# Optimization experiments

Hardware: AMD Instinct MI355X
Metric: run time of the kernel (lower is better)

The kernel has to match this reference:

```python
import jax, jax.numpy as jnp
import numpy as np

IN_F, ASS, OUT_F = 1024, 100000, 1024
P = 0.0005
NUM_ROUNDS = 24  # fixed replacement for the data-dependent convergence loop
TOTAL = IN_F + ASS + OUT_F


def _build_graph(seed=0):
    """Random digraph: input->assoc and assoc->(assoc|out) with prob P,
    plus guaranteed edges so the propagation_check of the original passes
    (every assoc node reachable, every output has an in-edge)."""
    rng = np.random.default_rng(seed)
    ass0, out0 = IN_F, IN_F + ASS
    n_ie = int(P * IN_F * ASS)
    ie_src = rng.integers(0, IN_F, n_ie)
    ie_dst = rng.integers(ass0, out0, n_ie)
    n_ae = int(P * ASS * (ASS + OUT_F))
    ae_src = rng.integers(ass0, out0, n_ae)
    ae_dst = rng.integers(ass0, out0 + OUT_F, n_ae)
    # guarantee reachability: assoc node j gets an in-edge from a random node < j
    g_dst = np.arange(ass0, out0)
    g_src = (rng.random(ASS) * g_dst).astype(np.int64)
    gi = g_src < IN_F
    ie_src = np.concatenate([ie_src, g_src[gi]])
    ie_dst = np.concatenate([ie_dst, g_dst[gi]])
    ae_src = np.concatenate([ae_src, g_src[~gi]])
    ae_dst = np.concatenate([ae_dst, g_dst[~gi]])
    # every output neuron gets at least one in-edge from a random assoc
    ae_src = np.concatenate([ae_src, rng.integers(ass0, out0, OUT_F)])
    ae_dst = np.concatenate([ae_dst, np.arange(out0, out0 + OUT_F)])
    return ie_src, ie_dst, ae_src, ae_dst


def setup_inputs() -> dict:
    key = jax.random.key(0)
    k1, k2, k3 = jax.random.split(key, 3)
    ie_src, ie_dst, ae_src, ae_dst = _build_graph()
    x = jax.random.normal(k1, (1, IN_F), jnp.float32)
    # nn.init.uniform_(w, -1, 1)
    input_weights = jax.random.uniform(k2, (len(ie_src),), jnp.float32, -1.0, 1.0)
    assoc_weights = jax.random.uniform(k3, (len(ae_src),), jnp.float32, -1.0, 1.0)
    return {
        'x': x,
        'input_weights': input_weights,
        'assoc_weights': assoc_weights,
        'in_edge_src': jnp.asarray(ie_src, jnp.int32),
        'in_edge_dst': jnp.asarray(ie_dst, jnp.int32),
        'ass_edge_src': jnp.asarray(ae_src, jnp.int32),
        'ass_edge_dst': jnp.asarray(ae_dst, jnp.int32),
    }


def _forward(x, input_weights, assoc_weights, in_edge_src, in_edge_dst,
             ass_edge_src, ass_edge_dst):
    idx = jnp.arange(TOTAL)
    is_assoc = (idx >= IN_F) & (idx < IN_F + ASS)
    # --- input phase: each input neuron i sends x[i]*w along its out-edges ---
    msgs = x[0][in_edge_src] * input_weights              # [E_in]
    mem = jax.ops.segment_sum(msgs, in_edge_dst, num_segments=TOTAL)
    recv = jax.ops.segment_sum(jnp.ones_like(in_edge_dst), in_edge_dst,
                               num_segments=TOTAL) > 0
    status = jnp.where(recv, 1, 0).astype(jnp.int32)      # 0=inactive,1=working,2=activated

    # --- synchronous wave propagation through associative neurons ---
    def step(carry, _):
        mem, status = carry
        fire = (status == 1) & is_assoc                    # working assoc neurons fire
        src_fire = fire[ass_edge_src]
        # forward_fn(memory, w) = activation(sum(memory)) * w  (tanh activation)
        vals = jnp.where(src_fire, jnp.tanh(mem[ass_edge_src]) * assoc_weights, 0.0)
        delta = jax.ops.segment_sum(vals, ass_edge_dst, num_segments=TOTAL)
        got = jax.ops.segment_sum(src_fire.astype(jnp.int32), ass_edge_dst,
                                  num_segments=TOTAL) > 0
        mem = jnp.where(fire, 0.0, mem) + delta            # fired neurons erase memory
        status = jnp.where(fire, 2, jnp.where(got & (status == 0), 1, status))
        return (mem, status), None

    (mem, status), _ = jax.lax.scan(step, (mem, status), None, length=NUM_ROUNDS)
    # --- output phase: Y[i] = activation(sum(memory)) * 1 ---
    return jnp.tanh(mem[IN_F + ASS:])


def reference(x, input_weights, assoc_weights, in_edge_src, in_edge_dst,
              ass_edge_src, ass_edge_dst):
    return _forward(x, input_weights, assoc_weights, in_edge_src, in_edge_dst,
                    ass_edge_src, ass_edge_dst)
```

## Files before the change

kernel.cpp:

```cpp
#include <hip/hip_runtime.h>

#define IN_F 1024
#define ASS 100000
#define OUT_F 1024
#define TOTAL (IN_F + ASS + OUT_F)
#define ASS0 IN_F
#define OUT0 (IN_F + ASS)
#define NDST (ASS + OUT_F)
#define NUM_ROUNDS 24

#define BIN_SZ 1024
#define BIN_SH 10
#define BIN_MK 1023
#define NBINS ((NDST + BIN_SZ - 1) / BIN_SZ)
#define NCON 512
#define CON_T 1024
#define SPLIT 8
#define NBM32 3136
#define TAIL_R 8

typedef int i4v __attribute__((ext_vector_type(4)));
typedef float f4v __attribute__((ext_vector_type(4)));
typedef unsigned int u2v __attribute__((ext_vector_type(2)));


__global__ __launch_bounds__(256) void kz(float* mem, u2v* ltv, int* flags,
                                          int* binA, int* binR, int* scur,
                                          unsigned* bm, int cap, int scap) {
  int i = blockIdx.x * 256 + threadIdx.x;
  int gs = gridDim.x * 256;
  u2v init;
  init.x = 255u;
  init.y = 0u;
  for (int k = i; k < TOTAL; k += gs) {
    mem[k] = 0.f;
    ltv[k] = init;
  }
  for (int k = i; k < NBINS; k += gs) {
    binA[k] = k * cap;
    binR[k] = (k + 1) * cap;
    scur[k] = k * scap;
  }
  for (int k = i; k < NBM32; k += gs) bm[k] = 0u;
  if (i < 32) flags[i] = 0;
}

__global__ __launch_bounds__(256) void ki(const float* __restrict__ x,
                                          const float* __restrict__ iw,
                                          const int* __restrict__ ies,
                                          const int* __restrict__ ied, int E_in,
                                          float* mem, unsigned int* ltv_raw,
                                          unsigned* bm) {
  int e = blockIdx.x * 256 + threadIdx.x;
  if (e < E_in) {
    int d = ied[e];
    atomicAdd(&mem[d], x[ies[e]] * iw[e]);
    ltv_raw[2 * d] = 0u;
    int b = d - ASS0;
    atomicOr(&bm[b >> 5], 1u << (b & 31));
  }
}

__global__ __launch_bounds__(CON_T) void kc(const int* __restrict__ aes,
                                            const int* __restrict__ aed,
                                            const float* __restrict__ aw,
                                            int E_a, int* binA, int* binR,
                                            const unsigned* __restrict__ bm,
                                            u2v* __restrict__ csr, float* mem,
                                            u2v* ltv) {
  for (int i = blockIdx.x * CON_T + (int)threadIdx.x; i < ASS;
       i += NCON * CON_T) {
    int node = ASS0 + i;
    u2v lt = ltv[node];
    if (lt.x == 0u) {
      lt.y = __float_as_uint(tanhf(mem[node]));
      ltv[node] = lt;
      mem[node] = 0.f;
    }
  }
  __shared__ unsigned sbm[NBM32];
  __shared__ int hA[2][NBINS], hR[2][NBINS];
  __shared__ int cA[NBINS], cR[NBINS];
  for (int k = threadIdx.x; k < NBM32; k += CON_T) sbm[k] = bm[k];
  for (int b = threadIdx.x; b < NBINS; b += CON_T) {
    hA[0][b] = 0;
    hA[1][b] = 0;
    hR[0][b] = 0;
    hR[1][b] = 0;
  }
  __syncthreads();
  int cp = (threadIdx.x >> 6) & 1;
  const i4v* aed4 = (const i4v*)aed;
  const i4v* aes4 = (const i4v*)aes;
  const f4v* aw4 = (const f4v*)aw;
  int nv4 = E_a >> 2;
  int chunk4 = (nv4 + NCON - 1) / NCON;
  int v0 = blockIdx.x * chunk4;
  int v1 = min(v0 + chunk4, nv4);
  int bv = v0 + (int)threadIdx.x;

  i4v dr0, dr1, dr2, sr0, sr1, sr2;
#pragma unroll
  for (int k = 0; k < 3; ++k) {
    int v = bv + k * CON_T;
    if (v < v1) {
      i4v d4 = aed4[v];
      i4v s4 = aes4[v];
      if (k == 0) { dr0 = d4; sr0 = s4; }
      if (k == 1) { dr1 = d4; sr1 = s4; }
      if (k == 2) { dr2 = d4; sr2 = s4; }
#pragma unroll
      for (int j = 0; j < 4; ++j) {
        int b = (d4[j] - ASS0) >> BIN_SH;
        int si = s4[j] - ASS0;
        bool a0 = (sbm[si >> 5] >> (si & 31)) & 1u;
        atomicAdd(a0 ? &hA[cp][b] : &hR[cp][b], 1);
      }
    }
  }
  for (int v = bv + 3 * CON_T; v < v1; v += CON_T) {
    i4v d4 = aed4[v];
    i4v s4 = aes4[v];
#pragma unroll
    for (int j = 0; j < 4; ++j) {
      int b = (d4[j] - ASS0) >> BIN_SH;
      int si = s4[j] - ASS0;
      bool a0 = (sbm[si >> 5] >> (si & 31)) & 1u;
      atomicAdd(a0 ? &hA[cp][b] : &hR[cp][b], 1);
    }
  }
  if (blockIdx.x == 0) {
    for (int e = (nv4 << 2) + (int)threadIdx.x; e < E_a; e += CON_T) {
      int b = (aed[e] - ASS0) >> BIN_SH;
      int si = aes[e] - ASS0;
      bool a0 = (sbm[si >> 5] >> (si & 31)) & 1u;
      atomicAdd(a0 ? &hA[cp][b] : &hR[cp][b], 1);
    }
  }
  __syncthreads();
  for (int b = threadIdx.x; b < NBINS; b += CON_T) {
    int ca = hA[0][b] + hA[1][b];
    int cr = hR[0][b] + hR[1][b];
    cA[b] = ca ? atomicAdd(&binA[b], ca) : 0;
    cR[b] = cr ? (atomicSub(&binR[b], cr) - cr) : 0;
  }
  __syncthreads();
#pragma unroll
  for (int k = 0; k < 3; ++k) {
    int v = bv + k * CON_T;
    if (v < v1) {
      i4v d4 = (k == 0) ? dr0 : (k == 1) ? dr1 : dr2;
      i4v s4 = (k == 0) ? sr0 : (k == 1) ? sr1 : sr2;
      f4v w4 = __builtin_nontemporal_load(&aw4[v]);
#pragma unroll
      for (int j = 0; j < 4; ++j) {
        int d = d4[j] - ASS0;
        int b = d >> BIN_SH;
        int si = s4[j] - ASS0;
        bool a0 = (sbm[si >> 5] >> (si & 31)) & 1u;
        int pos = atomicAdd(a0 ? &cA[b] : &cR[b], 1);
        u2v q;
        q.x = ((unsigned)s4[j] << BIN_SH) | (unsigned)(d & BIN_MK);
        q.y = __float_as_uint(w4[j]);
        csr[pos] = q;
      }
    }
  }
  for (int v = bv + 3 * CON_T; v < v1; v += CON_T) {
    i4v d4 = aed4[v];
    i4v s4 = aes4[v];
    f4v w4 = __builtin_nontemporal_load(&aw4[v]);
#pragma unroll
    for (int j = 0; j < 4; ++j) {
      int d = d4[j] - ASS0;
      int b = d >> BIN_SH;
      int si = s4[j] - ASS0;
      bool a0 = (sbm[si >> 5] >> (si & 31)) & 1u;
      int pos = atomicAdd(a0 ? &cA[b] : &cR[b], 1);
      u2v q;
      q.x = ((unsigned)s4[j] << BIN_SH) | (unsigned)(d & BIN_MK);
      q.y = __float_as_uint(w4[j]);
      csr[pos] = q;
    }
  }
  if (blockIdx.x == 0) {
    for (int e = (nv4 << 2) + (int)threadIdx.x; e < E_a; e += CON_T) {
      int d = aed[e] - ASS0;
      int b = d >> BIN_SH;
      int si = aes[e] - ASS0;
      bool a0 = (sbm[si >> 5] >> (si & 31)) & 1u;
      int pos = atomicAdd(a0 ? &cA[b] : &cR[b], 1);
      u2v q;
      q.x = ((unsigned)aes[e] << BIN_SH) | (unsigned)(d & BIN_MK);
      q.y = __float_as_uint(aw[e]);
      csr[pos] = q;
    }
  }
}

__global__ __launch_bounds__(256) void kRe(int r, int* flags,
                                           const int* __restrict__ binA,
                                           const int* __restrict__ binR,
                                           const u2v* __restrict__ csr,
                                           const u2v* __restrict__ ltv,
                                           float* __restrict__ gslice,
                                           char* __restrict__ gmask,
                                           u2v* __restrict__ ssur, int* scur,
                                           int cap, int scap) {
  if (r > 0 && flags[r] == 0) return;
  __shared__ float slice[BIN_SZ];
  __shared__ int smask[BIN_SZ];
  int tid = threadIdx.x;
  for (int i = tid; i < BIN_SZ; i += 256) {
    slice[i] = 0.f;
    smask[i] = 0;
  }
  __syncthreads();
  int bin = blockIdx.x >> 3;
  int sub = blockIdx.x & (SPLIT - 1);
  int e0 = (r == 0) ? bin * cap : binR[bin];
  int e1 = (r == 0) ? binA[bin] : (bin + 1) * cap;
  int len = e1 - e0;
  int chunk = (len + SPLIT - 1) / SPLIT;
  int s0 = e0 + sub * chunk;
  int s1 = min(s0 + chunk, e1);
#pragma unroll 4
  for (int e = s0 + tid; e < s1; e += 256) {
    u2v q = __builtin_nontemporal_load(&csr[e]);
    if (r == 0) {
      u2v lt = ltv[q.x >> BIN_SH];
      atomicAdd(&slice[q.x & BIN_MK],
                __uint_as_float(lt.y) * __uint_as_float(q.y));
      smask[q.x & BIN_MK] = 1;
    } else {
      u2v lt = ltv[q.x >> BIN_SH];
      if (lt.x == 1u) {
        atomicAdd(&slice[q.x & BIN_MK],
                  __uint_as_float(lt.y) * __uint_as_float(q.y));
        smask[q.x & BIN_MK] = 1;
      } else if (lt.x == 255u) {
        int pos = atomicAdd(&scur[bin], 1);
        if (pos < bin * scap + scap)
          ssur[pos] = q;
        else
          flags[30] = 1;
      }
    }
  }
  __syncthreads();
  int base = blockIdx.x * BIN_SZ;
  for (int i = tid; i < BIN_SZ; i += 256) {
    gslice[base + i] = slice[i];
    gmask[base + i] = (char)smask[i];
  }
}

__device__ __forceinline__ void mergeEpi(int r, int bin, int stride,
                                         const float* __restrict__ gslice,
                                         const char* __restrict__ gmask,
                                         float* __restrict__ mem,
                                         u2v* __restrict__ ltv, int* flags) {
  for (int t = threadIdx.x; t < BIN_SZ; t += stride) {
    float sv = 0.f;
    int mk = 0;
    int base = bin * SPLIT * BIN_SZ + t;
#pragma unroll
    for (int s = 0; s < SPLIT; ++s) {
      sv += gslice[base + s * BIN_SZ];
      mk |= (int)gmask[base + s * BIN_SZ];
    }
    int d = bin * BIN_SZ + t;
    if (d < NDST && mk) {
      int node = ASS0 + d;
      float nv = mem[node] + sv;
      u2v lt = ltv[node];
      if (lt.x == 255u) {
        u2v nl;
        nl.x = (unsigned)(r + 1);
        if (node < OUT0) {
          nl.y = __float_as_uint(tanhf(nv));
          ltv[node] = nl;
          mem[node] = 0.f;
          flags[r + 1] = 1;
        } else {
          nl.y = 0u;
          ltv[node] = nl;
          mem[node] = nv;
        }
      } else {
        mem[node] = nv;
      }
    }
  }
}

__global__ __launch_bounds__(1024) void kRn(int r, int* flags,
                                            const float* __restrict__ gslice,
                                            const char* __restrict__ gmask,
                                            float* __restrict__ mem,
                                            u2v* __restrict__ ltv) {
  if (r > 0 && flags[r] == 0) return;
  mergeEpi(r, blockIdx.x, 1024, gslice, gmask, mem, ltv, flags);
}

__global__ __launch_bounds__(1024) void kRt(int r, int* flags,
                                            const int* __restrict__ binR,
                                            const u2v* __restrict__ csr,
                                            const u2v* __restrict__ ssur,
                                            const int* __restrict__ scur,
                                            float* __restrict__ mem,
                                            u2v* __restrict__ ltv, int cap,
                                            int scap) {
  if (flags[r] == 0) return;
  __shared__ float slice[BIN_SZ];
  __shared__ int smask[BIN_SZ];
  int tid = threadIdx.x;
  int bin = blockIdx.x;
  slice[tid] = 0.f;
  smask[tid] = 0;
  __syncthreads();
  bool useS = (flags[30] == 0);
  int e0 = useS ? bin * scap : binR[bin];
  int e1 = useS ? min(scur[bin], bin * scap + scap) : (bin + 1) * cap;
  const u2v* E = useS ? ssur : csr;
  unsigned rl = (unsigned)r;
  for (int e = e0 + tid; e < e1; e += 1024) {
    u2v q = E[e];
    u2v lt = ltv[q.x >> BIN_SH];
    if (lt.x == rl) {
      atomicAdd(&slice[q.x & BIN_MK],
                __uint_as_float(lt.y) * __uint_as_float(q.y));
      smask[q.x & BIN_MK] = 1;
    }
  }
  __syncthreads();
  int d = bin * BIN_SZ + tid;
  if (d < NDST && smask[tid]) {
    int node = ASS0 + d;
    float nv = mem[node] + slice[tid];
    u2v lt = ltv[node];
    if (lt.x == 255u) {
      u2v nl;
      nl.x = (unsigned)(r + 1);
      if (node < OUT0) {
        nl.y = __float_as_uint(tanhf(nv));
        ltv[node] = nl;
        mem[node] = 0.f;
        flags[r + 1] = 1;
      } else {
        nl.y = 0u;
        ltv[node] = nl;
        mem[node] = nv;
      }
    } else {
      mem[node] = nv;
    }
  }
}

__global__ __launch_bounds__(256) void ko(const float* __restrict__ mem,
                                          float* __restrict__ out) {
  int i = blockIdx.x * 256 + threadIdx.x;
  if (i < OUT_F) out[i] = tanhf(mem[OUT0 + i]);
}


__global__ __launch_bounds__(256) void k_init(float* mem, float* delta,
                                              int* status, int* got) {
  int i = blockIdx.x * 256 + threadIdx.x;
  if (i < TOTAL) {
    mem[i] = 0.f;
    delta[i] = 0.f;
    status[i] = 0;
    got[i] = 0;
  }
}
__global__ __launch_bounds__(256) void k_input(const float* __restrict__ x,
                                               const float* __restrict__ w,
                                               const int* __restrict__ src,
                                               const int* __restrict__ dst,
                                               int n, float* mem, int* got) {
  for (int e = blockIdx.x * 256 + threadIdx.x; e < n; e += gridDim.x * 256) {
    atomicAdd(&mem[dst[e]], x[src[e]] * w[e]);
    got[dst[e]] = 1;
  }
}
__global__ __launch_bounds__(256) void k_status0(int* status, int* got) {
  int i = blockIdx.x * 256 + threadIdx.x;
  if (i < TOTAL) {
    status[i] = got[i] ? 1 : 0;
    got[i] = 0;
  }
}
__global__ __launch_bounds__(256) void k_edge(const float* __restrict__ w,
                                              const int* __restrict__ src,
                                              const int* __restrict__ dst,
                                              int n,
                                              const float* __restrict__ mem,
                                              const int* __restrict__ status,
                                              float* delta, int* got) {
  for (int e = blockIdx.x * 256 + threadIdx.x; e < n; e += gridDim.x * 256) {
    int s = src[e];
    if (status[s] == 1) {
      atomicAdd(&delta[dst[e]], tanhf(mem[s]) * w[e]);
      got[dst[e]] = 1;
    }
  }
}
__global__ __launch_bounds__(256) void k_update(float* mem, float* delta,
                                                int* status, int* got) {
  int i = blockIdx.x * 256 + threadIdx.x;
  if (i < TOTAL) {
    int st = status[i];
    bool fire = (st == 1) && (i >= ASS0) && (i < OUT0);
    float d = delta[i];
    mem[i] = fire ? d : (mem[i] + d);
    status[i] = fire ? 2 : ((got[i] && st == 0) ? 1 : st);
    delta[i] = 0.f;
    got[i] = 0;
  }
}

extern "C" void kernel_launch(void* const* d_in, const int* in_sizes, int n_in,
                              void* d_out, int out_size, void* d_ws,
                              size_t ws_size, hipStream_t stream) {
  const float* x = (const float*)d_in[0];
  const float* iw = (const float*)d_in[1];
  const float* aw = (const float*)d_in[2];
  const int* ies = (const int*)d_in[3];
  const int* ied = (const int*)d_in[4];
  const int* aes = (const int*)d_in[5];
  const int* aed = (const int*)d_in[6];
  int E_in = in_sizes[1];
  int E_a = in_sizes[2];
  float* out = (float*)d_out;
  char* ws = (char*)d_ws;

  int cap = (((E_a / NBINS) * 13) / 10 + 255) & ~255;
  int scap = cap / 4;

  size_t off_csr = 0;
  size_t off_ssur = off_csr + (size_t)NBINS * cap * 8;
  size_t off_ltv = off_ssur + (size_t)NBINS * scap * 8;
  size_t off_mem = off_ltv + (size_t)TOTAL * 8;
  size_t off_bA = off_mem + (size_t)TOTAL * 4;
  size_t off_bR = off_bA + (size_t)NBINS * 4;
  size_t off_scur = off_bR + (size_t)NBINS * 4;
  size_t off_flags = off_scur + (size_t)NBINS * 4;
  size_t off_bm = off_flags + 32 * 4;
  size_t off_gsl = off_bm + (size_t)NBM32 * 4;
  size_t off_gmk = off_gsl + (size_t)NBINS * SPLIT * BIN_SZ * 4;
  size_t need = off_gmk + (size_t)NBINS * SPLIT * BIN_SZ;

  if (ws_size >= need) {
    u2v* csr = (u2v*)(ws + off_csr);
    u2v* ssur = (u2v*)(ws + off_ssur);
    u2v* ltv = (u2v*)(ws + off_ltv);
    float* mem = (float*)(ws + off_mem);
    int* binA = (int*)(ws + off_bA);
    int* binR = (int*)(ws + off_bR);
    int* scur = (int*)(ws + off_scur);
    int* flags = (int*)(ws + off_flags);
    unsigned* bm = (unsigned*)(ws + off_bm);
    float* gslice = (float*)(ws + off_gsl);
    char* gmask = ws + off_gmk;

    kz<<<(TOTAL + 255) / 256, 256, 0, stream>>>(mem, ltv, flags, binA, binR,
                                                scur, bm, cap, scap);
    ki<<<(E_in + 255) / 256, 256, 0, stream>>>(x, iw, ies, ied, E_in, mem,
                                               (unsigned int*)ltv, bm);
    kc<<<NCON, CON_T, 0, stream>>>(aes, aed, aw, E_a, binA, binR, bm, csr,
                                   mem, ltv);

    for (int r = 0; r < 2; ++r) {
      kRe<<<NBINS * SPLIT, 256, 0, stream>>>(r, flags, binA, binR, csr, ltv,
                                             gslice, gmask, ssur, scur, cap,
                                             scap);
      kRn<<<NBINS, 1024, 0, stream>>>(r, flags, gslice, gmask, mem, ltv);
    }
    for (int r = 2; r < TAIL_R; ++r)
      kRt<<<NBINS, 1024, 0, stream>>>(r, flags, binR, csr, ssur, scur, mem,
                                      ltv, cap, scap);
    ko<<<(OUT_F + 255) / 256, 256, 0, stream>>>(mem, out);
    return;
  }

  float* mem = (float*)ws;
  float* delta = mem + TOTAL;
  int* status = (int*)(delta + TOTAL);
  int* got = status + TOTAL;
  const int nodeBlocks = (TOTAL + 255) / 256;
  k_init<<<nodeBlocks, 256, 0, stream>>>(mem, delta, status, got);
  int inBlocks = (E_in + 255) / 256;
  if (inBlocks > 1024) inBlocks = 1024;
  k_input<<<inBlocks, 256, 0, stream>>>(x, iw, ies, ied, E_in, mem, got);
  k_status0<<<nodeBlocks, 256, 0, stream>>>(status, got);
  int eBlocks = (E_a + 255) / 256;
  if (eBlocks > 2048) eBlocks = 2048;
  for (int r = 0; r < NUM_ROUNDS; ++r) {
    k_edge<<<eBlocks, 256, 0, stream>>>(aw, aes, aed, E_a, mem, status, delta,
                                        got);
    k_update<<<nodeBlocks, 256, 0, stream>>>(mem, delta, status, got);
  }
  ko<<<(OUT_F + 255) / 256, 256, 0, stream>>>(mem, out);
}
```

Baseline: 136.3 us.

## Stage CSR scatter in shared memory and write bins contiguously to global

The CSR construction kernel now buckets each block's edges into a shared-memory staging buffer, ordered by (active/rest, bin). A block-wide prefix scan gives local offsets, and the staged entries are then copied to global memory in contiguous per-bin runs instead of being scattered one at a time. The grid size is now chosen at launch so that each block's chunk fits the staging buffer. The shared bitmap copy and the duplicated histogram copies were removed, so bitmap lookups now read global memory directly. The extra barriers, the binary search per output element and the heavy LDS use could lower occupancy, in exchange for better-coalesced writes.

```diff
diff --git a/kernel.cpp b/kernel.cpp
--- a/kernel.cpp
+++ b/kernel.cpp
@@ -13,8 +13,8 @@
 #define BIN_SH 10
 #define BIN_MK 1023
 #define NBINS ((NDST + BIN_SZ - 1) / BIN_SZ)
-#define NCON 512
 #define CON_T 1024
+#define STAGE_E 7424
 #define SPLIT 8
 #define NBM32 3136
 #define TAIL_R 8
@@ -68,8 +68,8 @@
                                             const unsigned* __restrict__ bm,
                                             u2v* __restrict__ csr, float* mem,
                                             u2v* ltv) {
-  for (int i = blockIdx.x * CON_T + (int)threadIdx.x; i < ASS;
-       i += NCON * CON_T) {
+  int tid = threadIdx.x;
+  for (int i = blockIdx.x * CON_T + tid; i < ASS; i += gridDim.x * CON_T) {
     int node = ASS0 + i;
     u2v lt = ltv[node];
     if (lt.x == 0u) {
@@ -78,123 +78,118 @@
       mem[node] = 0.f;
     }
   }
-  __shared__ unsigned sbm[NBM32];
-  __shared__ int hA[2][NBINS], hR[2][NBINS];
-  __shared__ int cA[NBINS], cR[NBINS];
-  for (int k = threadIdx.x; k < NBM32; k += CON_T) sbm[k] = bm[k];
-  for (int b = threadIdx.x; b < NBINS; b += CON_T) {
-    hA[0][b] = 0;
-    hA[1][b] = 0;
-    hR[0][b] = 0;
-    hR[1][b] = 0;
-  }
-  __syncthreads();
-  int cp = (threadIdx.x >> 6) & 1;
+  __shared__ u2v stage[STAGE_E];
+  __shared__ int hAB[2 * NBINS];
+  __shared__ int pref[2 * NBINS + 1];
+  __shared__ int gb[2 * NBINS];
+  __shared__ int curs[2 * NBINS];
+  __shared__ int sc[256];
+  for (int k = tid; k < 2 * NBINS; k += CON_T) hAB[k] = 0;
+  __syncthreads();
   const i4v* aed4 = (const i4v*)aed;
   const i4v* aes4 = (const i4v*)aes;
   const f4v* aw4 = (const f4v*)aw;
   int nv4 = E_a >> 2;
-  int chunk4 = (nv4 + NCON - 1) / NCON;
+  int chunk4 = (nv4 + gridDim.x - 1) / gridDim.x;
   int v0 = blockIdx.x * chunk4;
   int v1 = min(v0 + chunk4, nv4);
-  int bv = v0 + (int)threadIdx.x;
-
-  i4v dr0, dr1, dr2, sr0, sr1, sr2;
+  int bv = v0 + tid;
+  i4v dr0, dr1, sr0, sr1;
 #pragma unroll
-  for (int k = 0; k < 3; ++k) {
+  for (int k = 0; k < 2; ++k) {
     int v = bv + k * CON_T;
     if (v < v1) {
       i4v d4 = aed4[v];
       i4v s4 = aes4[v];
-      if (k == 0) { dr0 = d4; sr0 = s4; }
-      if (k == 1) { dr1 = d4; sr1 = s4; }
-      if (k == 2) { dr2 = d4; sr2 = s4; }
+      if (k == 0) {
+        dr0 = d4;
+        sr0 = s4;
+      } else {
+        dr1 = d4;
+        sr1 = s4;
+      }
 #pragma unroll
       for (int j = 0; j < 4; ++j) {
         int b = (d4[j] - ASS0) >> BIN_SH;
         int si = s4[j] - ASS0;
-        bool a0 = (sbm[si >> 5] >> (si & 31)) & 1u;
-        atomicAdd(a0 ? &hA[cp][b] : &hR[cp][b], 1);
+        bool a0 = (bm[si >> 5] >> (si & 31)) & 1u;
+        atomicAdd(&hAB[a0 ? b : NBINS + b], 1);
       }
     }
   }
-  for (int v = bv + 3 * CON_T; v < v1; v += CON_T) {
-    i4v d4 = aed4[v];
-    i4v s4 = aes4[v];
+  __syncthreads();
+  int vlen = (tid < 2 * NBINS) ? hAB[tid] : 0;
+  if (tid < 256) sc[tid] = vlen;
+  __syncthreads();
+  for (int off = 1; off < 256; off <<= 1) {
+    int t = 0;
+    if (tid < 256 && tid >= off) t = sc[tid - off];
+    __syncthreads();
+    if (tid < 256) sc[tid] += t;
+    __syncthreads();
+  }
+  if (tid < 2 * NBINS) {
+    int ex = sc[tid] - vlen;
+    pref[tid] = ex;
+    curs[tid] = ex;
+    if (vlen) {
+      if (tid < NBINS)
+        gb[tid] = atomicAdd(&binA[tid], vlen);
+      else
+        gb[tid] = atomicSub(&binR[tid - NBINS], vlen) - vlen;
+    } else {
+      gb[tid] = 0;
+    }
+  }
+  if (tid == 0) pref[2 * NBINS] = sc[2 * NBINS - 1];
+  __syncthreads();
 #pragma unroll
-    for (int j = 0; j < 4; ++j) {
-      int b = (d4[j] - ASS0) >> BIN_SH;
-      int si = s4[j] - ASS0;
-      bool a0 = (sbm[si >> 5] >> (si & 31)) & 1u;
-      atomicAdd(a0 ? &hA[cp][b] : &hR[cp][b], 1);
-    }
-  }
-  if (blockIdx.x == 0) {
-    for (int e = (nv4 << 2) + (int)threadIdx.x; e < E_a; e += CON_T) {
-      int b = (aed[e] - ASS0) >> BIN_SH;
-      int si = aes[e] - ASS0;
-      bool a0 = (sbm[si >> 5] >> (si & 31)) & 1u;
-      atomicAdd(a0 ? &hA[cp][b] : &hR[cp][b], 1);
-    }
-  }
-  __syncthreads();
-  for (int b = threadIdx.x; b < NBINS; b += CON_T) {
-    int ca = hA[0][b] + hA[1][b];
-    int cr = hR[0][b] + hR[1][b];
-    cA[b] = ca ? atomicAdd(&binA[b], ca) : 0;
-    cR[b] = cr ? (atomicSub(&binR[b], cr) - cr) : 0;
-  }
-  __syncthreads();
-#pragma unroll
-  for (int k = 0; k < 3; ++k) {
+  for (int k = 0; k < 2; ++k) {
     int v = bv + k * CON_T;
     if (v < v1) {
-      i4v d4 = (k == 0) ? dr0 : (k == 1) ? dr1 : dr2;
-      i4v s4 = (k == 0) ? sr0 : (k == 1) ? sr1 : sr2;
+      i4v d4 = (k == 0) ? dr0 : dr1;
+      i4v s4 = (k == 0) ? sr0 : sr1;
       f4v w4 = __builtin_nontemporal_load(&aw4[v]);
 #pragma unroll
       for (int j = 0; j < 4; ++j) {
         int d = d4[j] - ASS0;
         int b = d >> BIN_SH;
         int si = s4[j] - ASS0;
-        bool a0 = (sbm[si >> 5] >> (si & 31)) & 1u;
-        int pos = atomicAdd(a0 ? &cA[b] : &cR[b], 1);
+        bool a0 = (bm[si >> 5] >> (si & 31)) & 1u;
+        int p = atomicAdd(&curs[a0 ? b : NBINS + b], 1);
         u2v q;
         q.x = ((unsigned)s4[j] << BIN_SH) | (unsigned)(d & BIN_MK);
         q.y = __float_as_uint(w4[j]);
-        csr[pos] = q;
+        stage[p] = q;
       }
     }
   }
-  for (int v = bv + 3 * CON_T; v < v1; v += CON_T) {
-    i4v d4 = aed4[v];
-    i4v s4 = aes4[v];
-    f4v w4 = __builtin_nontemporal_load(&aw4[v]);
-#pragma unroll
-    for (int j = 0; j < 4; ++j) {
-      int d = d4[j] - ASS0;
-      int b = d >> BIN_SH;
-      int si = s4[j] - ASS0;
-      bool a0 = (sbm[si >> 5] >> (si & 31)) & 1u;
-      int pos = atomicAdd(a0 ? &cA[b] : &cR[b], 1);
-      u2v q;
-      q.x = ((unsigned)s4[j] << BIN_SH) | (unsigned)(d & BIN_MK);
-      q.y = __float_as_uint(w4[j]);
-      csr[pos] = q;
-    }
-  }
   if (blockIdx.x == 0) {
-    for (int e = (nv4 << 2) + (int)threadIdx.x; e < E_a; e += CON_T) {
+    for (int e = (nv4 << 2) + tid; e < E_a; e += CON_T) {
       int d = aed[e] - ASS0;
       int b = d >> BIN_SH;
       int si = aes[e] - ASS0;
-      bool a0 = (sbm[si >> 5] >> (si & 31)) & 1u;
-      int pos = atomicAdd(a0 ? &cA[b] : &cR[b], 1);
+      bool a0 = (bm[si >> 5] >> (si & 31)) & 1u;
+      int pos = a0 ? atomicAdd(&binA[b], 1) : (atomicSub(&binR[b], 1) - 1);
       u2v q;
       q.x = ((unsigned)aes[e] << BIN_SH) | (unsigned)(d & BIN_MK);
       q.y = __float_as_uint(aw[e]);
       csr[pos] = q;
     }
+  }
+  __syncthreads();
+  int total = pref[2 * NBINS];
+  for (int t = tid; t < total; t += CON_T) {
+    int lo = 0, hi = 2 * NBINS - 1;
+#pragma unroll
+    for (int it = 0; it < 8; ++it) {
+      int mid = (lo + hi + 1) >> 1;
+      if (pref[mid] <= t)
+        lo = mid;
+      else
+        hi = mid - 1;
+    }
+    csr[gb[lo] + (t - pref[lo])] = stage[t];
   }
 }
 
@@ -469,7 +464,11 @@
                                                 scur, bm, cap, scap);
     ki<<<(E_in + 255) / 256, 256, 0, stream>>>(x, iw, ies, ied, E_in, mem,
                                                (unsigned int*)ltv, bm);
-    kc<<<NCON, CON_T, 0, stream>>>(aes, aed, aw, E_a, binA, binR, bm, csr,
+    int nv4 = E_a >> 2;
+    int ncon = (E_a + STAGE_E - 1) / STAGE_E;
+    if (ncon < 512) ncon = 512;
+    while ((((nv4 + ncon - 1) / ncon) << 2) > STAGE_E) ++ncon;
+    kc<<<ncon, CON_T, 0, stream>>>(aes, aed, aw, E_a, binA, binR, bm, csr,
                                    mem, ltv);
 
     for (int r = 0; r < 2; ++r) {
```

Result: faster. 132.0 us (-3.1%).
